# Optimization experiments

Measured on AMD Instinct MI355X. Metric: run time of the kernel, lower is better.

The kernel has to match this reference:

```python
import jax, jax.numpy as jnp
import numpy as np

TEMPERATURE = 0.07
N, D = 8192, 1024
NUM_CLASSES = 1000


def setup_inputs() -> dict:
    key = jax.random.key(0)
    k1, k2 = jax.random.split(key)
    vectors = jax.random.normal(k1, (N, D), dtype=jnp.float32)
    labels = jax.random.randint(k2, (N,), 0, NUM_CLASSES, dtype=jnp.int32)
    return {"vectors": vectors, "labels": labels}


def reference(vectors, labels):
    # cosine similarity matrix, scaled by temperature
    a = vectors / jnp.linalg.norm(vectors, axis=1, keepdims=True)
    sim = jnp.matmul(a, a.T) / TEMPERATURE  # [N, N]
    n = sim.shape[0]
    eye = jnp.eye(n, dtype=bool)

    # per-row logsumexp over off-diagonal entries (diagonal removed)
    denom = jax.nn.logsumexp(jnp.where(eye, -jnp.inf, sim), axis=1)  # [N]

    # same-label mask, excluding self
    same = (labels[:, None] == labels[None, :]) & ~eye  # [N, N]
    cnt = jnp.sum(same, axis=1)  # [N] number of positives per anchor

    # numerator_j = -mean(sim[j, positives]); rows with no positives skipped
    pos_sum = jnp.sum(jnp.where(same, sim, 0.0), axis=1)
    numerator = -pos_sum / jnp.maximum(cnt, 1).astype(sim.dtype)

    per_row = jnp.where(cnt > 0, denom + numerator, 0.0)
    return jnp.sum(per_row)
```

## Files before the change

kernel.cpp:

```cpp
#include <hip/hip_runtime.h>
#include <hip/hip_bf16.h>
#include <stdint.h>

#define N_ROWS 8192
#define DIM    1024
#define INV_T  14.2857142857142857f
#define SCL    (INV_T / 1024.0f)

#define BM   128
#define RPB  512
#define TKB  64
#define NTILE  (N_ROWS / BM)
#define NSLICE (2 * NTILE)
#define NKT    8
#define NPAIR  2080
#define PER_XCD (NPAIR / 8)

typedef int   i32x4 __attribute__((ext_vector_type(4)));
typedef int   i32x8 __attribute__((ext_vector_type(8)));
typedef float f32x4 __attribute__((ext_vector_type(4)));

__device__ __forceinline__ unsigned e2m1(float y) {
    const float a = fabsf(y);
    unsigned c = a < 0.25f ? 0u : a < 0.75f ? 1u : a < 1.25f ? 2u :
                 a < 1.75f ? 3u : a < 2.5f  ? 4u : a < 3.5f  ? 5u :
                 a < 5.0f  ? 6u : 7u;
    return c | (y < 0.f ? 8u : 0u);
}

__global__ __launch_bounds__(256) void norm_kernel(
    const float* __restrict__ V, unsigned char* __restrict__ A4)
{
    const int wid  = threadIdx.x >> 6;
    const int lane = threadIdx.x & 63;
    const int row  = blockIdx.x * 4 + wid;

    const float4* vp = (const float4*)(V + (size_t)row * DIM);
    float4 v[4];
    float ss = 0.f;
    #pragma unroll
    for (int i = 0; i < 4; ++i) {
        v[i] = vp[lane + i * 64];
        ss += v[i].x*v[i].x + v[i].y*v[i].y + v[i].z*v[i].z + v[i].w*v[i].w;
    }
    #pragma unroll
    for (int off = 1; off < 64; off <<= 1) ss += __shfl_xor(ss, off, 64);
    const float inv = 32.0f / sqrtf(ss);

    unsigned short op[4];
    #pragma unroll
    for (int i = 0; i < 4; ++i) {
        const unsigned e0 = e2m1(v[i].x * inv), e1 = e2m1(v[i].y * inv);
        const unsigned e2 = e2m1(v[i].z * inv), e3 = e2m1(v[i].w * inv);
        op[i] = (unsigned short)(e0 | (e1 << 4) | (e2 << 8) | (e3 << 12));
    }
    unsigned char* dst = A4 + (size_t)row * RPB;
    #pragma unroll
    for (int i = 0; i < 4; ++i)
        ((unsigned short*)dst)[lane + i * 64] = op[i];
}

__global__ __launch_bounds__(256, 3) void sim_kernel(
    const unsigned char* __restrict__ A4, const int* __restrict__ labels,
    float* __restrict__ psum, float* __restrict__ ppos, float* __restrict__ pcnt)
{
    __shared__ __align__(16) unsigned char As[2][BM * TKB];
    __shared__ __align__(16) unsigned char Bs[2][BM * TKB];

    const int b = blockIdx.x;
    const int v = (b & 7) * PER_XCD + (b >> 3);
    int rem = v, RT = 0, rowsz = 36 + 7 * 64;
    while (rem >= rowsz) { rem -= rowsz; ++RT; rowsz -= 64; }
    int rt, ct;
    if (rem < 36) {
        int i = 0, left = 8;
        while (rem >= left) { rem -= left; ++i; --left; }
        rt = RT * 8 + i;  ct = RT * 8 + i + rem;
    } else {
        const int o  = rem - 36;
        const int CT = RT + 1 + (o >> 6);
        const int w  = o & 63;
        rt = RT * 8 + (w >> 3);
        ct = CT * 8 + (w & 7);
    }
    const bool isDiag = (rt == ct);

    const int tid  = threadIdx.x;
    const int lane = tid & 63;
    const int wid  = tid >> 6;
    const int wr   = wid >> 1;
    const int wc   = wid & 1;

    const int rbase = rt * BM;
    const int cbase = ct * BM;

    const int t = lane >> 4;
    const int j = lane & 15;

    const int rowq = rbase + wr * 64 + (t << 2);
    const int col0 = cbase + wc * 64 + j;

    int labr[16];
    #pragma unroll
    for (int m = 0; m < 4; ++m)
        #pragma unroll
        for (int r = 0; r < 4; ++r)
            labr[m * 4 + r] = labels[rowq + m * 16 + r];
    int labc[4];
    #pragma unroll
    for (int n = 0; n < 4; ++n) labc[n] = labels[col0 + n * 16];

    f32x4 acc[4][4];
    #pragma unroll
    for (int m = 0; m < 4; ++m)
        #pragma unroll
        for (int n = 0; n < 4; ++n)
            acc[m][n] = (f32x4){0.f, 0.f, 0.f, 0.f};

    #define STAGE(buf, kt)                                                         \
    {                                                                              \
        const int kbase = (kt) * TKB;                                              \
        _Pragma("unroll")                                                          \
        for (int i = 0; i < 2; ++i) {                                              \
            const int c    = i * 256 + tid;                                        \
            const int rowc = c >> 2;                                               \
            const int kcs  = (c & 3) ^ (rowc & 3);                                 \
            const unsigned char* gA = A4 + (size_t)(rbase + rowc) * RPB + kbase + kcs * 16; \
            const unsigned char* gB = A4 + (size_t)(cbase + rowc) * RPB + kbase + kcs * 16; \
            const int ldsOff = i * 4096 + wid * 1024;          \
            __builtin_amdgcn_global_load_lds(                                      \
                (const __attribute__((address_space(1))) void*)gA,                 \
                (__attribute__((address_space(3))) void*)(As[buf] + ldsOff),       \
                16, 0, 0);                                                         \
            __builtin_amdgcn_global_load_lds(                                      \
                (const __attribute__((address_space(1))) void*)gB,                 \
                (__attribute__((address_space(3))) void*)(Bs[buf] + ldsOff),       \
                16, 0, 0);                                                         \
        }                                                                          \
    }

    const i32x4 Z4 = (i32x4){0, 0, 0, 0};

    STAGE(0, 0);
    __syncthreads();

    int cur = 0;
    for (int kt = 0; kt < NKT; ++kt) {
        i32x8 a8[4], b8[4];
        #pragma unroll
        for (int m = 0; m < 4; ++m) {
            const int rowa = wr * 64 + m * 16 + j;
            const int ph   = ((t ^ (rowa & 3)) << 4);
            i32x4 q = *(const i32x4*)(As[cur] + rowa * TKB + ph);
            a8[m] = __builtin_shufflevector(q, Z4, 0, 1, 2, 3, 4, 5, 6, 7);
        }
        #pragma unroll
        for (int n = 0; n < 4; ++n) {
            const int rowb = wc * 64 + n * 16 + j;
            const int ph   = ((t ^ (rowb & 3)) << 4);
            i32x4 q = *(const i32x4*)(Bs[cur] + rowb * TKB + ph);
            b8[n] = __builtin_shufflevector(q, Z4, 0, 1, 2, 3, 4, 5, 6, 7);
        }

        if (kt + 1 < NKT) STAGE(cur ^ 1, kt + 1);

        __builtin_amdgcn_s_setprio(1);
        #pragma unroll
        for (int m = 0; m < 4; ++m)
            #pragma unroll
            for (int n = 0; n < 4; ++n)
                acc[m][n] = __builtin_amdgcn_mfma_scale_f32_16x16x128_f8f6f4(
                    a8[m], b8[n], acc[m][n],
                    4 , 4 ,
                    0, 0x7F , 0, 0x7F );
        __builtin_amdgcn_s_setprio(0);

        __syncthreads();
        cur ^= 1;
    }

    float sum_p[16], pos_p[16], cnt_p[16];
    #pragma unroll
    for (int i = 0; i < 16; ++i) { sum_p[i] = 0.f; pos_p[i] = 0.f; cnt_p[i] = 0.f; }
    float csum[4], cpos[4], ccnt[4];
    #pragma unroll
    for (int n = 0; n < 4; ++n) { csum[n] = 0.f; cpos[n] = 0.f; ccnt[n] = 0.f; }

    if (isDiag) {
        #pragma unroll
        for (int m = 0; m < 4; ++m)
            #pragma unroll
            for (int n = 0; n < 4; ++n) {
                const int gcol = col0 + n * 16;
                #pragma unroll
                for (int r = 0; r < 4; ++r) {
                    const float s    = acc[m][n][r] * SCL;
                    const int   i16  = m * 4 + r;
                    const int   grow = rowq + m * 16 + r;
                    const bool  diag = (grow == gcol);
                    sum_p[i16] += diag ? 0.f : __expf(s);
                    if ((labr[i16] == labc[n]) && !diag) {
                        pos_p[i16] += s; cnt_p[i16] += 1.f;
                    }
                }
            }
    } else {
        #pragma unroll
        for (int m = 0; m < 4; ++m)
            #pragma unroll
            for (int n = 0; n < 4; ++n) {
                #pragma unroll
                for (int r = 0; r < 4; ++r) {
                    const float s   = acc[m][n][r] * SCL;
                    const int   i16 = m * 4 + r;
                    const float e   = __expf(s);
                    sum_p[i16] += e;
                    csum[n]    += e;
                    if (labr[i16] == labc[n]) {
                        pos_p[i16] += s; cnt_p[i16] += 1.f;
                        cpos[n]    += s; ccnt[n]    += 1.f;
                    }
                }
            }
    }

    #pragma unroll
    for (int bb = 1; bb <= 8; bb <<= 1) {
        const bool hi = (j & bb) != 0;
        #pragma unroll
        for (int k = 0; k < 8; ++k) {
            if (k < 16 / (2 * bb)) {
                const float eK = hi ? sum_p[2*k+1] : sum_p[2*k];
                const float eS = hi ? sum_p[2*k]   : sum_p[2*k+1];
                sum_p[k] = eK + __shfl_xor(eS, bb, 16);
                const float pK = hi ? pos_p[2*k+1] : pos_p[2*k];
                const float pS = hi ? pos_p[2*k]   : pos_p[2*k+1];
                pos_p[k] = pK + __shfl_xor(pS, bb, 16);
                const float cK = hi ? cnt_p[2*k+1] : cnt_p[2*k];
                const float cS = hi ? cnt_p[2*k]   : cnt_p[2*k+1];
                cnt_p[k] = cK + __shfl_xor(cS, bb, 16);
            }
        }
    }
    {
        const int rowS = rowq + ((j >> 2) << 4) + (j & 3);
        const size_t idx = (size_t)(ct * 2 + wc) * N_ROWS + rowS;
        psum[idx] = sum_p[0];
        ppos[idx] = pos_p[0];
        pcnt[idx] = cnt_p[0];
    }

    if (!isDiag) {
        #pragma unroll
        for (int n = 0; n < 4; ++n) {
            float se = csum[n], pp = cpos[n], cc = ccnt[n];
            se += __shfl_xor(se, 16, 64); se += __shfl_xor(se, 32, 64);
            pp += __shfl_xor(pp, 16, 64); pp += __shfl_xor(pp, 32, 64);
            cc += __shfl_xor(cc, 16, 64); cc += __shfl_xor(cc, 32, 64);
            if (lane < 16) {
                const int gcol = col0 + n * 16;
                const size_t idx = (size_t)(rt * 2 + wr) * N_ROWS + gcol;
                psum[idx] = se;
                ppos[idx] = pp;
                pcnt[idx] = cc;
            }
        }
    }
}

__global__ __launch_bounds__(1024) void finalize_kernel(
    const float* __restrict__ psum, const float* __restrict__ ppos,
    const float* __restrict__ pcnt, float* __restrict__ out)
{
    __shared__ float sh0[1024], sh1[1024], sh2[1024];
    __shared__ float w4[4];

    const int tid = threadIdx.x;
    const int r   = tid & 255;
    const int q   = tid >> 8;
    const int row = blockIdx.x * 256 + r;

    float s = 0.f, p = 0.f, c = 0.f;
    #pragma unroll 8
    for (int sl = q * 32; sl < q * 32 + 32; ++sl) {
        const size_t idx = (size_t)sl * N_ROWS + row;
        s += psum[idx];
        p += ppos[idx];
        c += pcnt[idx];
    }
    sh0[tid] = s; sh1[tid] = p; sh2[tid] = c;
    __syncthreads();

    float per = 0.f;
    if (tid < 256) {
        s = sh0[tid] + sh0[tid + 256] + sh0[tid + 512] + sh0[tid + 768];
        p = sh1[tid] + sh1[tid + 256] + sh1[tid + 512] + sh1[tid + 768];
        c = sh2[tid] + sh2[tid + 256] + sh2[tid + 512] + sh2[tid + 768];
        per = (c > 0.f) ? (logf(s) - p / c) : 0.f;
    }
    #pragma unroll
    for (int off = 32; off > 0; off >>= 1) per += __shfl_down(per, off, 64);
    if (tid < 256 && (tid & 63) == 0) w4[tid >> 6] = per;
    __syncthreads();
    if (tid == 0)
        atomicAdd(out, w4[0] + w4[1] + w4[2] + w4[3]);
}

extern "C" void kernel_launch(void* const* d_in, const int* in_sizes, int n_in,
                              void* d_out, int out_size, void* d_ws, size_t ws_size,
                              hipStream_t stream) {
    const float* V      = (const float*)d_in[0];
    const int*   labels = (const int*)d_in[1];
    float*       out    = (float*)d_out;

    unsigned char* A4 = (unsigned char*)d_ws;
    char* base = (char*)d_ws + (size_t)N_ROWS * RPB;
    float* psum = (float*)(base);
    float* ppos = (float*)(base + (size_t)NSLICE * N_ROWS * 4);
    float* pcnt = (float*)(base + (size_t)NSLICE * N_ROWS * 8);

    hipMemsetAsync(out, 0, sizeof(float), stream);
    norm_kernel<<<N_ROWS / 4, 256, 0, stream>>>(V, A4);
    sim_kernel<<<NPAIR, 256, 0, stream>>>(A4, labels, psum, ppos, pcnt);
    finalize_kernel<<<N_ROWS / 256, 1024, 0, stream>>>(psum, ppos, pcnt, out);
}
```

Measured before the change: 59.69 us.

## Derive positive counts from label histogram and pack partial sums as float2

Removes the per-element positive-count accumulation and its shuffles and stores from the similarity kernel. The finalize kernel instead builds a shared-memory label histogram and takes each count as hist[label]-1. Partial sum and positive sums are written as one float2, and exp is computed with exp2 using a prefolded scale (SCL applied later for positives). Other changes: the memset is folded into norm_kernel, staging addresses are precomputed, and the conditional positive add becomes a select. The trade-off is that every finalize block rebuilds the full 8192-label histogram with LDS atomics.

After: 52.45 us. -12.1%, faster.

```diff
diff --git a/kernel.cpp b/kernel.cpp
--- a/kernel.cpp
+++ b/kernel.cpp
@@ -6,6 +6,8 @@
 #define DIM    1024
 #define INV_T  14.2857142857142857f
 #define SCL    (INV_T / 1024.0f)
+#define C1     (SCL * 1.44269504088896f)
+#define NCLS   1000
 
 #define BM   128
 #define RPB  512
@@ -29,8 +31,11 @@
 }
 
 __global__ __launch_bounds__(256) void norm_kernel(
-    const float* __restrict__ V, unsigned char* __restrict__ A4)
+    const float* __restrict__ V, unsigned char* __restrict__ A4,
+    float* __restrict__ out)
 {
+    if (blockIdx.x == 0 && threadIdx.x == 0) out[0] = 0.f;
+
     const int wid  = threadIdx.x >> 6;
     const int lane = threadIdx.x & 63;
     const int row  = blockIdx.x * 4 + wid;
@@ -62,7 +67,7 @@
 
 __global__ __launch_bounds__(256, 3) void sim_kernel(
     const unsigned char* __restrict__ A4, const int* __restrict__ labels,
-    float* __restrict__ psum, float* __restrict__ ppos, float* __restrict__ pcnt)
+    float2* __restrict__ pp)
 {
     __shared__ __align__(16) unsigned char As[2][BM * TKB];
     __shared__ __align__(16) unsigned char Bs[2][BM * TKB];
@@ -117,23 +122,27 @@
         for (int n = 0; n < 4; ++n)
             acc[m][n] = (f32x4){0.f, 0.f, 0.f, 0.f};
 
-    #define STAGE(buf, kt)                                                         \
+    const unsigned char* sgA[2];
+    const unsigned char* sgB[2];
+    #pragma unroll
+    for (int i = 0; i < 2; ++i) {
+        const int c    = i * 256 + tid;
+        const int rowc = c >> 2;
+        const int kcs  = (c & 3) ^ (rowc & 3);
+        sgA[i] = A4 + (size_t)(rbase + rowc) * RPB + kcs * 16;
+        sgB[i] = A4 + (size_t)(cbase + rowc) * RPB + kcs * 16;
+    }
+    #define STAGE(buf, kOff)                                                       \
     {                                                                              \
-        const int kbase = (kt) * TKB;                                              \
         _Pragma("unroll")                                                          \
         for (int i = 0; i < 2; ++i) {                                              \
-            const int c    = i * 256 + tid;                                        \
-            const int rowc = c >> 2;                                               \
-            const int kcs  = (c & 3) ^ (rowc & 3);                                 \
-            const unsigned char* gA = A4 + (size_t)(rbase + rowc) * RPB + kbase + kcs * 16; \
-            const unsigned char* gB = A4 + (size_t)(cbase + rowc) * RPB + kbase + kcs * 16; \
             const int ldsOff = i * 4096 + wid * 1024;          \
             __builtin_amdgcn_global_load_lds(                                      \
-                (const __attribute__((address_space(1))) void*)gA,                 \
+                (const __attribute__((address_space(1))) void*)(sgA[i] + (kOff)),  \
                 (__attribute__((address_space(3))) void*)(As[buf] + ldsOff),       \
                 16, 0, 0);                                                         \
             __builtin_amdgcn_global_load_lds(                                      \
-                (const __attribute__((address_space(1))) void*)gB,                 \
+                (const __attribute__((address_space(1))) void*)(sgB[i] + (kOff)),  \
                 (__attribute__((address_space(3))) void*)(Bs[buf] + ldsOff),       \
                 16, 0, 0);                                                         \
         }                                                                          \
@@ -162,7 +171,7 @@
             b8[n] = __builtin_shufflevector(q, Z4, 0, 1, 2, 3, 4, 5, 6, 7);
         }
 
-        if (kt + 1 < NKT) STAGE(cur ^ 1, kt + 1);
+        if (kt + 1 < NKT) STAGE(cur ^ 1, (kt + 1) * TKB);
 
         __builtin_amdgcn_s_setprio(1);
         #pragma unroll
@@ -179,12 +188,12 @@
         cur ^= 1;
     }
 
-    float sum_p[16], pos_p[16], cnt_p[16];
-    #pragma unroll
-    for (int i = 0; i < 16; ++i) { sum_p[i] = 0.f; pos_p[i] = 0.f; cnt_p[i] = 0.f; }
-    float csum[4], cpos[4], ccnt[4];
-    #pragma unroll
-    for (int n = 0; n < 4; ++n) { csum[n] = 0.f; cpos[n] = 0.f; ccnt[n] = 0.f; }
+    float sum_p[16], pos_p[16];
+    #pragma unroll
+    for (int i = 0; i < 16; ++i) { sum_p[i] = 0.f; pos_p[i] = 0.f; }
+    float csum[4], cpos[4];
+    #pragma unroll
+    for (int n = 0; n < 4; ++n) { csum[n] = 0.f; cpos[n] = 0.f; }
 
     if (isDiag) {
         #pragma unroll
@@ -194,14 +203,13 @@
                 const int gcol = col0 + n * 16;
                 #pragma unroll
                 for (int r = 0; r < 4; ++r) {
-                    const float s    = acc[m][n][r] * SCL;
+                    const float a    = acc[m][n][r];
                     const int   i16  = m * 4 + r;
                     const int   grow = rowq + m * 16 + r;
                     const bool  diag = (grow == gcol);
-                    sum_p[i16] += diag ? 0.f : __expf(s);
-                    if ((labr[i16] == labc[n]) && !diag) {
-                        pos_p[i16] += s; cnt_p[i16] += 1.f;
-                    }
+                    const float e    = diag ? 0.f : __builtin_amdgcn_exp2f(a * C1);
+                    sum_p[i16] += e;
+                    if ((labr[i16] == labc[n]) && !diag) pos_p[i16] += a;
                 }
             }
     } else {
@@ -211,15 +219,14 @@
             for (int n = 0; n < 4; ++n) {
                 #pragma unroll
                 for (int r = 0; r < 4; ++r) {
-                    const float s   = acc[m][n][r] * SCL;
+                    const float a   = acc[m][n][r];
                     const int   i16 = m * 4 + r;
-                    const float e   = __expf(s);
+                    const float e   = __builtin_amdgcn_exp2f(a * C1);
+                    const float pa  = (labr[i16] == labc[n]) ? a : 0.f;
                     sum_p[i16] += e;
+                    pos_p[i16] += pa;
                     csum[n]    += e;
-                    if (labr[i16] == labc[n]) {
-                        pos_p[i16] += s; cnt_p[i16] += 1.f;
-                        cpos[n]    += s; ccnt[n]    += 1.f;
-                    }
+                    cpos[n]    += pa;
                 }
             }
     }
@@ -236,67 +243,62 @@
                 const float pK = hi ? pos_p[2*k+1] : pos_p[2*k];
                 const float pS = hi ? pos_p[2*k]   : pos_p[2*k+1];
                 pos_p[k] = pK + __shfl_xor(pS, bb, 16);
-                const float cK = hi ? cnt_p[2*k+1] : cnt_p[2*k];
-                const float cS = hi ? cnt_p[2*k]   : cnt_p[2*k+1];
-                cnt_p[k] = cK + __shfl_xor(cS, bb, 16);
             }
         }
     }
     {
         const int rowS = rowq + ((j >> 2) << 4) + (j & 3);
-        const size_t idx = (size_t)(ct * 2 + wc) * N_ROWS + rowS;
-        psum[idx] = sum_p[0];
-        ppos[idx] = pos_p[0];
-        pcnt[idx] = cnt_p[0];
+        pp[(size_t)(ct * 2 + wc) * N_ROWS + rowS] = make_float2(sum_p[0], pos_p[0]);
     }
 
     if (!isDiag) {
         #pragma unroll
         for (int n = 0; n < 4; ++n) {
-            float se = csum[n], pp = cpos[n], cc = ccnt[n];
+            float se = csum[n], pq = cpos[n];
             se += __shfl_xor(se, 16, 64); se += __shfl_xor(se, 32, 64);
-            pp += __shfl_xor(pp, 16, 64); pp += __shfl_xor(pp, 32, 64);
-            cc += __shfl_xor(cc, 16, 64); cc += __shfl_xor(cc, 32, 64);
+            pq += __shfl_xor(pq, 16, 64); pq += __shfl_xor(pq, 32, 64);
             if (lane < 16) {
                 const int gcol = col0 + n * 16;
-                const size_t idx = (size_t)(rt * 2 + wr) * N_ROWS + gcol;
-                psum[idx] = se;
-                ppos[idx] = pp;
-                pcnt[idx] = cc;
+                pp[(size_t)(rt * 2 + wr) * N_ROWS + gcol] = make_float2(se, pq);
             }
         }
     }
 }
 
 __global__ __launch_bounds__(1024) void finalize_kernel(
-    const float* __restrict__ psum, const float* __restrict__ ppos,
-    const float* __restrict__ pcnt, float* __restrict__ out)
+    const float2* __restrict__ pp, const int* __restrict__ labels,
+    float* __restrict__ out)
 {
-    __shared__ float sh0[1024], sh1[1024], sh2[1024];
+    __shared__ int   hist[NCLS];
+    __shared__ float sh0[1024], sh1[1024];
     __shared__ float w4[4];
 
     const int tid = threadIdx.x;
+
+    for (int i = tid; i < NCLS; i += 1024) hist[i] = 0;
+    __syncthreads();
+    for (int i = tid; i < N_ROWS; i += 1024) atomicAdd(&hist[labels[i]], 1);
+
     const int r   = tid & 255;
     const int q   = tid >> 8;
     const int row = blockIdx.x * 256 + r;
 
-    float s = 0.f, p = 0.f, c = 0.f;
+    float s = 0.f, p = 0.f;
     #pragma unroll 8
     for (int sl = q * 32; sl < q * 32 + 32; ++sl) {
-        const size_t idx = (size_t)sl * N_ROWS + row;
-        s += psum[idx];
-        p += ppos[idx];
-        c += pcnt[idx];
-    }
-    sh0[tid] = s; sh1[tid] = p; sh2[tid] = c;
+        const float2 v = pp[(size_t)sl * N_ROWS + row];
+        s += v.x;
+        p += v.y;
+    }
+    sh0[tid] = s; sh1[tid] = p;
     __syncthreads();
 
     float per = 0.f;
     if (tid < 256) {
         s = sh0[tid] + sh0[tid + 256] + sh0[tid + 512] + sh0[tid + 768];
         p = sh1[tid] + sh1[tid + 256] + sh1[tid + 512] + sh1[tid + 768];
-        c = sh2[tid] + sh2[tid + 256] + sh2[tid + 512] + sh2[tid + 768];
-        per = (c > 0.f) ? (logf(s) - p / c) : 0.f;
+        const int c = hist[labels[row]] - 1;
+        per = (c > 0) ? (logf(s) - (SCL * p) / (float)c) : 0.f;
     }
     #pragma unroll
     for (int off = 32; off > 0; off >>= 1) per += __shfl_down(per, off, 64);
@@ -314,13 +316,9 @@
     float*       out    = (float*)d_out;
 
     unsigned char* A4 = (unsigned char*)d_ws;
-    char* base = (char*)d_ws + (size_t)N_ROWS * RPB;
-    float* psum = (float*)(base);
-    float* ppos = (float*)(base + (size_t)NSLICE * N_ROWS * 4);
-    float* pcnt = (float*)(base + (size_t)NSLICE * N_ROWS * 8);
-
-    hipMemsetAsync(out, 0, sizeof(float), stream);
-    norm_kernel<<<N_ROWS / 4, 256, 0, stream>>>(V, A4);
-    sim_kernel<<<NPAIR, 256, 0, stream>>>(A4, labels, psum, ppos, pcnt);
-    finalize_kernel<<<N_ROWS / 256, 1024, 0, stream>>>(psum, ppos, pcnt, out);
-}
+    float2* pp = (float2*)((char*)d_ws + (size_t)N_ROWS * RPB);
+
+    norm_kernel<<<N_ROWS / 4, 256, 0, stream>>>(V, A4, out);
+    sim_kernel<<<NPAIR, 256, 0, stream>>>(A4, labels, pp);
+    finalize_kernel<<<N_ROWS / 256, 1024, 0, stream>>>(pp, labels, out);
+}
```
